# Performance work log

Measured on AMD Instinct MI355X. Metric: run time of the kernel, lower is better.

Reference implementation:

```python
import jax, jax.numpy as jnp
import numpy as np

B, T, U = 2048, 200, 128


def setup_inputs() -> dict:
    key = jax.random.key(0)
    ks = jax.random.split(key, 9)
    s = 1.0 / np.sqrt(U)
    inp = {
        "interest_states": jax.random.normal(ks[0], (B, T, U), dtype=jnp.float32),
        "attention_scores": jax.random.uniform(ks[1], (B, T, 1), dtype=jnp.float32),
        "W_xu": jax.random.normal(ks[2], (U, U), dtype=jnp.float32) * s,
        "b_xu": jnp.zeros((U,), dtype=jnp.float32),
        "W_hu": jax.random.normal(ks[3], (U, U), dtype=jnp.float32) * s,
        "b_hu": jnp.zeros((U,), dtype=jnp.float32),
        "W_xr": jax.random.normal(ks[4], (U, U), dtype=jnp.float32) * s,
        "b_xr": jnp.zeros((U,), dtype=jnp.float32),
        "W_hr": jax.random.normal(ks[5], (U, U), dtype=jnp.float32) * s,
        "b_hr": jnp.zeros((U,), dtype=jnp.float32),
        "W_xc": jax.random.normal(ks[6], (U, U), dtype=jnp.float32) * s,
        "b_xc": jnp.zeros((U,), dtype=jnp.float32),
        "W_hc": jax.random.normal(ks[7], (U, U), dtype=jnp.float32) * s,
        "b_hc": jnp.zeros((U,), dtype=jnp.float32),
    }
    return inp


def reference(interest_states, attention_scores, W_xu, b_xu, W_hu, b_hu,
              W_xr, b_xr, W_hr, b_hr, W_xc, b_xc, W_hc, b_hc):
    # Precompute input-side projections for all timesteps (batched GEMMs).
    xu = jnp.einsum('btu,uv->btv', interest_states, W_xu) + b_xu  # [B,T,U]
    xr = jnp.einsum('btu,uv->btv', interest_states, W_xr) + b_xr
    xc = jnp.einsum('btu,uv->btv', interest_states, W_xc) + b_xc
    # Time-major for scan: [T,B,U] / [T,B,1]
    xu_t = jnp.swapaxes(xu, 0, 1)
    xr_t = jnp.swapaxes(xr, 0, 1)
    xc_t = jnp.swapaxes(xc, 0, 1)
    att_t = jnp.swapaxes(attention_scores, 0, 1)  # [T,B,1]

    def step(h, inp):
        xu_i, xr_i, xc_i, a_i = inp
        u = jax.nn.sigmoid(xu_i + h @ W_hu + b_hu)       # update gate [B,U]
        r = jax.nn.sigmoid(xr_i + h @ W_hr + b_hr)       # reset gate  [B,U]
        c = jnp.tanh(xc_i + (r * h) @ W_hc + b_hc)       # candidate   [B,U]
        au = a_i * u                                     # attention-scaled update gate
        h_new = (1.0 - au) * h + au * c
        return h_new, None

    h0 = jnp.zeros((interest_states.shape[0], W_hu.shape[0]), dtype=interest_states.dtype)
    h_final, _ = jax.lax.scan(step, h0, (xu_t, xr_t, xc_t, att_t))
    return h_final  # [B,U]
```

## Files before the change

### kernel.cpp

```cpp
#include <hip/hip_runtime.h>
#include <hip/hip_bf16.h>

#define B_  2048
#define T_  200
#define U_  128
#define NB  8
#define PITCH 136

typedef __attribute__((ext_vector_type(8))) short short8;
typedef __attribute__((ext_vector_type(4))) short short4_t;
typedef __attribute__((ext_vector_type(4))) float f32x4;

static __device__ inline short f2bf(float f) {
  union { float f; unsigned u; } v; v.f = f;
  unsigned r = v.u + 0x7FFFu + ((v.u >> 16) & 1u);
  return (short)(r >> 16);
}
static __device__ inline float sigm(float x) {
  return __builtin_amdgcn_rcpf(1.0f + __builtin_amdgcn_exp2f(x * -1.44269504088896340736f));
}
static __device__ inline float tanh_fast(float x) {
  return 1.0f - 2.0f * __builtin_amdgcn_rcpf(1.0f + __builtin_amdgcn_exp2f(x * 2.88539008177792681472f));
}

__global__ void prep_weights(const float* __restrict__ Wxu, const float* __restrict__ Wxr,
                             const float* __restrict__ Wxc, const float* __restrict__ Whu,
                             const float* __restrict__ Whr, const float* __restrict__ Whc,
                             short* __restrict__ out) {
  const int m = blockIdx.x >> 7;
  const int n = blockIdx.x & 127;
  const int k = threadIdx.x;
  const float* Wp;
  switch (m) {
    case 0: Wp = Wxu; break; case 1: Wp = Wxr; break; case 2: Wp = Wxc; break;
    case 3: Wp = Whu; break; case 4: Wp = Whr; break; default: Wp = Whc; break;
  }
  out[(m * 128 + n) * 128 + k] = f2bf(Wp[k * 128 + n]);
}

__global__ __launch_bounds__(256, 1) void augru_scan(
    const float* __restrict__ IS, const float* __restrict__ ATT,
    const float* __restrict__ bxu, const float* __restrict__ bhu,
    const float* __restrict__ bxr, const float* __restrict__ bhr,
    const float* __restrict__ bxc, const float* __restrict__ bhc,
    const short* __restrict__ WT, float* __restrict__ out) {
  __shared__ short h_bf[16][PITCH];
  __shared__ short x_bf[16][PITCH];
  __shared__ short rh_bf[16][PITCH];
  __shared__ float att_s[T_][NB];

  const int tid  = threadIdx.x;
  const int w    = tid >> 6;
  const int l    = tid & 63;
  const int l15  = l & 15;
  const int lg   = l >> 4;
  const int b0   = blockIdx.x * NB;
  const int colb = w * 32;

  for (int i = tid; i < 16 * PITCH / 2; i += 256) {
    ((int*)h_bf)[i] = 0; ((int*)x_bf)[i] = 0; ((int*)rh_bf)[i] = 0;
  }
  for (int i = tid; i < T_ * NB; i += 256) {
    int r = i / T_, t = i % T_;
    att_s[t][r] = ATT[(size_t)(b0 + r) * T_ + t];
  }
  const int prow = tid >> 5;
  const int pc4  = (tid & 31) * 4;
  {
    f32x4 xv = *(const f32x4*)(IS + ((size_t)(b0 + prow) * T_ + 0) * U_ + pc4);
    short4_t xb;
    xb[0] = f2bf(xv[0]); xb[1] = f2bf(xv[1]); xb[2] = f2bf(xv[2]); xb[3] = f2bf(xv[3]);
    *(short4_t*)&x_bf[prow][pc4] = xb;
  }
  short8 Wf[6][2][4];
#pragma unroll
  for (int m = 0; m < 6; ++m)
#pragma unroll
    for (int nf = 0; nf < 2; ++nf)
#pragma unroll
      for (int kf = 0; kf < 4; ++kf) {
        const int col = colb + nf * 16 + l15;
        Wf[m][nf][kf] = *(const short8*)(WT + ((m * 128 + col) * 128 + kf * 32 + lg * 8));
      }
  float bu[2], br[2], bc[2];
#pragma unroll
  for (int nf = 0; nf < 2; ++nf) {
    const int col = colb + nf * 16 + l15;
    bu[nf] = bxu[col] + bhu[col];
    br[nf] = bxr[col] + bhr[col];
    bc[nf] = bxc[col] + bhc[col];
  }

  const f32x4 fz = {0.0f, 0.0f, 0.0f, 0.0f};
  f32x4 hreg[2]; hreg[0] = fz; hreg[1] = fz;
  float ureg[2][4];

  for (int t = 0; t < T_; ++t) {
    __syncthreads();
    short8 xa[4], ha[4];
#pragma unroll
    for (int kf = 0; kf < 4; ++kf) {
      xa[kf] = *(const short8*)&x_bf[l15][kf * 32 + lg * 8];
      ha[kf] = *(const short8*)&h_bf[l15][kf * 32 + lg * 8];
    }
    const int tn = (t < T_ - 1) ? t + 1 : t;
    f32x4 xnext = *(const f32x4*)(IS + ((size_t)(b0 + prow) * T_ + tn) * U_ + pc4);

    f32x4 axu[2], axr[2], axc[2], ahu[2], ahr[2];
#pragma unroll
    for (int nf = 0; nf < 2; ++nf) { axu[nf] = fz; axr[nf] = fz; axc[nf] = fz; ahu[nf] = fz; ahr[nf] = fz; }
#pragma unroll
    for (int nf = 0; nf < 2; ++nf)
#pragma unroll
      for (int kf = 0; kf < 4; ++kf) {
        axu[nf] = __builtin_amdgcn_mfma_f32_16x16x32_bf16(xa[kf], Wf[0][nf][kf], axu[nf], 0, 0, 0);
        axr[nf] = __builtin_amdgcn_mfma_f32_16x16x32_bf16(xa[kf], Wf[1][nf][kf], axr[nf], 0, 0, 0);
        axc[nf] = __builtin_amdgcn_mfma_f32_16x16x32_bf16(xa[kf], Wf[2][nf][kf], axc[nf], 0, 0, 0);
        ahu[nf] = __builtin_amdgcn_mfma_f32_16x16x32_bf16(ha[kf], Wf[3][nf][kf], ahu[nf], 0, 0, 0);
        ahr[nf] = __builtin_amdgcn_mfma_f32_16x16x32_bf16(ha[kf], Wf[4][nf][kf], ahr[nf], 0, 0, 0);
      }
#pragma unroll
    for (int nf = 0; nf < 2; ++nf)
#pragma unroll
      for (int rg = 0; rg < 4; ++rg) {
        float ug = sigm(axu[nf][rg] + ahu[nf][rg] + bu[nf]);
        float rr = sigm(axr[nf][rg] + ahr[nf][rg] + br[nf]);
        ureg[nf][rg] = ug;
        rh_bf[lg * 4 + rg][colb + nf * 16 + l15] = f2bf(rr * hreg[nf][rg]);
      }
    __syncthreads();
    short8 ra[4];
#pragma unroll
    for (int kf = 0; kf < 4; ++kf) ra[kf] = *(const short8*)&rh_bf[l15][kf * 32 + lg * 8];
    f32x4 ahc[2]; ahc[0] = fz; ahc[1] = fz;
#pragma unroll
    for (int nf = 0; nf < 2; ++nf)
#pragma unroll
      for (int kf = 0; kf < 4; ++kf)
        ahc[nf] = __builtin_amdgcn_mfma_f32_16x16x32_bf16(ra[kf], Wf[5][nf][kf], ahc[nf], 0, 0, 0);
    f32x4 a4 = *(const f32x4*)&att_s[t][(lg & 1) * 4];
#pragma unroll
    for (int nf = 0; nf < 2; ++nf)
#pragma unroll
      for (int rg = 0; rg < 4; ++rg) {
        float cc = tanh_fast(axc[nf][rg] + ahc[nf][rg] + bc[nf]);
        float au = a4[rg] * ureg[nf][rg];
        float hv = (1.0f - au) * hreg[nf][rg] + au * cc;
        hreg[nf][rg] = hv;
        h_bf[lg * 4 + rg][colb + nf * 16 + l15] = f2bf(hv);
      }
    {
      short4_t xb;
      xb[0] = f2bf(xnext[0]); xb[1] = f2bf(xnext[1]); xb[2] = f2bf(xnext[2]); xb[3] = f2bf(xnext[3]);
      *(short4_t*)&x_bf[prow][pc4] = xb;
    }
  }
#pragma unroll
  for (int nf = 0; nf < 2; ++nf)
#pragma unroll
    for (int rg = 0; rg < 4; ++rg) {
      const int row = lg * 4 + rg;
      if (row < NB) out[(size_t)(b0 + row) * U_ + colb + nf * 16 + l15] = hreg[nf][rg];
    }
}

extern "C" void kernel_launch(void* const* d_in, const int* in_sizes, int n_in,
                              void* d_out, int out_size, void* d_ws, size_t ws_size,
                              hipStream_t stream) {
  const float* IS  = (const float*)d_in[0];
  const float* ATT = (const float*)d_in[1];
  const float* Wxu = (const float*)d_in[2];  const float* bxu = (const float*)d_in[3];
  const float* Whu = (const float*)d_in[4];  const float* bhu = (const float*)d_in[5];
  const float* Wxr = (const float*)d_in[6];  const float* bxr = (const float*)d_in[7];
  const float* Whr = (const float*)d_in[8];  const float* bhr = (const float*)d_in[9];
  const float* Wxc = (const float*)d_in[10]; const float* bxc = (const float*)d_in[11];
  const float* Whc = (const float*)d_in[12]; const float* bhc = (const float*)d_in[13];
  short* WT  = (short*)d_ws;
  float* OUT = (float*)d_out;

  prep_weights<<<dim3(6 * 128), dim3(128), 0, stream>>>(Wxu, Wxr, Wxc, Whu, Whr, Whc, WT);
  augru_scan<<<dim3(B_ / NB), dim3(256), 0, stream>>>(IS, ATT, bxu, bhu, bxr, bhr, bxc, bhc, WT, OUT);
}
```

Before: 527.1 us.

## Split scan columns across 8 waves per block and coalesce weight prep reads

The recurrent scan now runs with 512 threads (8 waves) per block, so each wave owns 16 output columns instead of 32. This halves the MFMA chain and weight registers per wave and lets two blocks share a CU, aiming to hide the serial per-step latency better. The cost is more waves taking part in each per-step barrier, and x staging uses narrower 2-element loads. prep_weights also swaps its index mapping so consecutive threads read contiguous weight rows, which coalesces its global reads but makes its writes strided.

```diff
diff --git a/kernel.cpp b/kernel.cpp
--- a/kernel.cpp
+++ b/kernel.cpp
@@ -8,8 +8,9 @@
 #define PITCH 136
 
 typedef __attribute__((ext_vector_type(8))) short short8;
-typedef __attribute__((ext_vector_type(4))) short short4_t;
+typedef __attribute__((ext_vector_type(2))) short short2_t;
 typedef __attribute__((ext_vector_type(4))) float f32x4;
+typedef __attribute__((ext_vector_type(2))) float f32x2;
 
 static __device__ inline short f2bf(float f) {
   union { float f; unsigned u; } v; v.f = f;
@@ -28,8 +29,8 @@
                              const float* __restrict__ Whr, const float* __restrict__ Whc,
                              short* __restrict__ out) {
   const int m = blockIdx.x >> 7;
-  const int n = blockIdx.x & 127;
-  const int k = threadIdx.x;
+  const int k = blockIdx.x & 127;
+  const int n = threadIdx.x;
   const float* Wp;
   switch (m) {
     case 0: Wp = Wxu; break; case 1: Wp = Wxr; break; case 2: Wp = Wxc; break;
@@ -38,7 +39,7 @@
   out[(m * 128 + n) * 128 + k] = f2bf(Wp[k * 128 + n]);
 }
 
-__global__ __launch_bounds__(256, 1) void augru_scan(
+__global__ __launch_bounds__(512, 2) void augru_scan(
     const float* __restrict__ IS, const float* __restrict__ ATT,
     const float* __restrict__ bxu, const float* __restrict__ bhu,
     const float* __restrict__ bxr, const float* __restrict__ bhr,
@@ -55,45 +56,36 @@
   const int l15  = l & 15;
   const int lg   = l >> 4;
   const int b0   = blockIdx.x * NB;
-  const int colb = w * 32;
+  const int colb = w * 16;
+  const int col  = colb + l15;
 
-  for (int i = tid; i < 16 * PITCH / 2; i += 256) {
+  for (int i = tid; i < 16 * PITCH / 2; i += 512) {
     ((int*)h_bf)[i] = 0; ((int*)x_bf)[i] = 0; ((int*)rh_bf)[i] = 0;
   }
-  for (int i = tid; i < T_ * NB; i += 256) {
+  for (int i = tid; i < T_ * NB; i += 512) {
     int r = i / T_, t = i % T_;
     att_s[t][r] = ATT[(size_t)(b0 + r) * T_ + t];
   }
-  const int prow = tid >> 5;
-  const int pc4  = (tid & 31) * 4;
+  const int prow = w;
+  const int pc2  = (tid & 63) * 2;
   {
-    f32x4 xv = *(const f32x4*)(IS + ((size_t)(b0 + prow) * T_ + 0) * U_ + pc4);
-    short4_t xb;
-    xb[0] = f2bf(xv[0]); xb[1] = f2bf(xv[1]); xb[2] = f2bf(xv[2]); xb[3] = f2bf(xv[3]);
-    *(short4_t*)&x_bf[prow][pc4] = xb;
+    f32x2 xv = *(const f32x2*)(IS + ((size_t)(b0 + prow) * T_ + 0) * U_ + pc2);
+    short2_t xb; xb[0] = f2bf(xv[0]); xb[1] = f2bf(xv[1]);
+    *(short2_t*)&x_bf[prow][pc2] = xb;
   }
-  short8 Wf[6][2][4];
+  short8 Wf[6][4];
 #pragma unroll
   for (int m = 0; m < 6; ++m)
 #pragma unroll
-    for (int nf = 0; nf < 2; ++nf)
-#pragma unroll
-      for (int kf = 0; kf < 4; ++kf) {
-        const int col = colb + nf * 16 + l15;
-        Wf[m][nf][kf] = *(const short8*)(WT + ((m * 128 + col) * 128 + kf * 32 + lg * 8));
-      }
-  float bu[2], br[2], bc[2];
-#pragma unroll
-  for (int nf = 0; nf < 2; ++nf) {
-    const int col = colb + nf * 16 + l15;
-    bu[nf] = bxu[col] + bhu[col];
-    br[nf] = bxr[col] + bhr[col];
-    bc[nf] = bxc[col] + bhc[col];
-  }
+    for (int kf = 0; kf < 4; ++kf)
+      Wf[m][kf] = *(const short8*)(WT + ((m * 128 + col) * 128 + kf * 32 + lg * 8));
+  const float bu = bxu[col] + bhu[col];
+  const float br = bxr[col] + bhr[col];
+  const float bc = bxc[col] + bhc[col];
 
   const f32x4 fz = {0.0f, 0.0f, 0.0f, 0.0f};
-  f32x4 hreg[2]; hreg[0] = fz; hreg[1] = fz;
-  float ureg[2][4];
+  f32x4 hreg = fz;
+  float ureg[4];
 
   for (int t = 0; t < T_; ++t) {
     __syncthreads();
@@ -104,64 +96,51 @@
       ha[kf] = *(const short8*)&h_bf[l15][kf * 32 + lg * 8];
     }
     const int tn = (t < T_ - 1) ? t + 1 : t;
-    f32x4 xnext = *(const f32x4*)(IS + ((size_t)(b0 + prow) * T_ + tn) * U_ + pc4);
+    f32x2 xnext = *(const f32x2*)(IS + ((size_t)(b0 + prow) * T_ + tn) * U_ + pc2);
 
-    f32x4 axu[2], axr[2], axc[2], ahu[2], ahr[2];
+    f32x4 axu = fz, axr = fz, axc = fz, ahu = fz, ahr = fz;
 #pragma unroll
-    for (int nf = 0; nf < 2; ++nf) { axu[nf] = fz; axr[nf] = fz; axc[nf] = fz; ahu[nf] = fz; ahr[nf] = fz; }
+    for (int kf = 0; kf < 4; ++kf) {
+      axu = __builtin_amdgcn_mfma_f32_16x16x32_bf16(xa[kf], Wf[0][kf], axu, 0, 0, 0);
+      axr = __builtin_amdgcn_mfma_f32_16x16x32_bf16(xa[kf], Wf[1][kf], axr, 0, 0, 0);
+      axc = __builtin_amdgcn_mfma_f32_16x16x32_bf16(xa[kf], Wf[2][kf], axc, 0, 0, 0);
+      ahu = __builtin_amdgcn_mfma_f32_16x16x32_bf16(ha[kf], Wf[3][kf], ahu, 0, 0, 0);
+      ahr = __builtin_amdgcn_mfma_f32_16x16x32_bf16(ha[kf], Wf[4][kf], ahr, 0, 0, 0);
+    }
 #pragma unroll
-    for (int nf = 0; nf < 2; ++nf)
-#pragma unroll
-      for (int kf = 0; kf < 4; ++kf) {
-        axu[nf] = __builtin_amdgcn_mfma_f32_16x16x32_bf16(xa[kf], Wf[0][nf][kf], axu[nf], 0, 0, 0);
-        axr[nf] = __builtin_amdgcn_mfma_f32_16x16x32_bf16(xa[kf], Wf[1][nf][kf], axr[nf], 0, 0, 0);
-        axc[nf] = __builtin_amdgcn_mfma_f32_16x16x32_bf16(xa[kf], Wf[2][nf][kf], axc[nf], 0, 0, 0);
-        ahu[nf] = __builtin_amdgcn_mfma_f32_16x16x32_bf16(ha[kf], Wf[3][nf][kf], ahu[nf], 0, 0, 0);
-        ahr[nf] = __builtin_amdgcn_mfma_f32_16x16x32_bf16(ha[kf], Wf[4][nf][kf], ahr[nf], 0, 0, 0);
-      }
-#pragma unroll
-    for (int nf = 0; nf < 2; ++nf)
-#pragma unroll
-      for (int rg = 0; rg < 4; ++rg) {
-        float ug = sigm(axu[nf][rg] + ahu[nf][rg] + bu[nf]);
-        float rr = sigm(axr[nf][rg] + ahr[nf][rg] + br[nf]);
-        ureg[nf][rg] = ug;
-        rh_bf[lg * 4 + rg][colb + nf * 16 + l15] = f2bf(rr * hreg[nf][rg]);
-      }
+    for (int rg = 0; rg < 4; ++rg) {
+      float ug = sigm(axu[rg] + ahu[rg] + bu);
+      float rr = sigm(axr[rg] + ahr[rg] + br);
+      ureg[rg] = ug;
+      rh_bf[lg * 4 + rg][col] = f2bf(rr * hreg[rg]);
+    }
     __syncthreads();
     short8 ra[4];
 #pragma unroll
     for (int kf = 0; kf < 4; ++kf) ra[kf] = *(const short8*)&rh_bf[l15][kf * 32 + lg * 8];
-    f32x4 ahc[2]; ahc[0] = fz; ahc[1] = fz;
+    f32x4 ahc = fz;
 #pragma unroll
-    for (int nf = 0; nf < 2; ++nf)
-#pragma unroll
-      for (int kf = 0; kf < 4; ++kf)
-        ahc[nf] = __builtin_amdgcn_mfma_f32_16x16x32_bf16(ra[kf], Wf[5][nf][kf], ahc[nf], 0, 0, 0);
+    for (int kf = 0; kf < 4; ++kf)
+      ahc = __builtin_amdgcn_mfma_f32_16x16x32_bf16(ra[kf], Wf[5][kf], ahc, 0, 0, 0);
     f32x4 a4 = *(const f32x4*)&att_s[t][(lg & 1) * 4];
 #pragma unroll
-    for (int nf = 0; nf < 2; ++nf)
-#pragma unroll
-      for (int rg = 0; rg < 4; ++rg) {
-        float cc = tanh_fast(axc[nf][rg] + ahc[nf][rg] + bc[nf]);
-        float au = a4[rg] * ureg[nf][rg];
-        float hv = (1.0f - au) * hreg[nf][rg] + au * cc;
-        hreg[nf][rg] = hv;
-        h_bf[lg * 4 + rg][colb + nf * 16 + l15] = f2bf(hv);
-      }
+    for (int rg = 0; rg < 4; ++rg) {
+      float cc = tanh_fast(axc[rg] + ahc[rg] + bc);
+      float au = a4[rg] * ureg[rg];
+      float hv = (1.0f - au) * hreg[rg] + au * cc;
+      hreg[rg] = hv;
+      h_bf[lg * 4 + rg][col] = f2bf(hv);
+    }
     {
-      short4_t xb;
-      xb[0] = f2bf(xnext[0]); xb[1] = f2bf(xnext[1]); xb[2] = f2bf(xnext[2]); xb[3] = f2bf(xnext[3]);
-      *(short4_t*)&x_bf[prow][pc4] = xb;
+      short2_t xb; xb[0] = f2bf(xnext[0]); xb[1] = f2bf(xnext[1]);
+      *(short2_t*)&x_bf[prow][pc2] = xb;
     }
   }
 #pragma unroll
-  for (int nf = 0; nf < 2; ++nf)
-#pragma unroll
-    for (int rg = 0; rg < 4; ++rg) {
-      const int row = lg * 4 + rg;
-      if (row < NB) out[(size_t)(b0 + row) * U_ + colb + nf * 16 + l15] = hreg[nf][rg];
-    }
+  for (int rg = 0; rg < 4; ++rg) {
+    const int row = lg * 4 + rg;
+    if (row < NB) out[(size_t)(b0 + row) * U_ + col] = hreg[rg];
+  }
 }
 
 extern "C" void kernel_launch(void* const* d_in, const int* in_sizes, int n_in,
@@ -179,5 +158,5 @@
   float* OUT = (float*)d_out;
 
   prep_weights<<<dim3(6 * 128), dim3(128), 0, stream>>>(Wxu, Wxr, Wxc, Whu, Whr, Whc, WT);
-  augru_scan<<<dim3(B_ / NB), dim3(256), 0, stream>>>(IS, ATT, bxu, bhu, bxr, bhr, bxc, bhc, WT, OUT);
+  augru_scan<<<dim3(B_ / NB), dim3(512), 0, stream>>>(IS, ATT, bxu, bhu, bxr, bhr, bxc, bhc, WT, OUT);
 }
```

Result: faster. 450.9 us (-14.5%).
